# Kernel optimization log

Measured on AMD Instinct MI355X. Metric: run time of the kernel, lower is better.

The kernel has to match this reference:

```python
import jax, jax.numpy as jnp
import numpy as np

CODEBOOK_SIZE = 1024
EMBED_DIM = 256
DECAY = 0.99
EPS = 1e-05


def setup_inputs() -> dict:
    key = jax.random.key(0)
    k_in, k_emb = jax.random.split(key)
    inputs = jax.random.normal(k_in, (128, 16, 16, EMBED_DIM), dtype=jnp.float32)
    embedding = jax.random.normal(k_emb, (CODEBOOK_SIZE, EMBED_DIM), dtype=jnp.float32)
    cluster_size = jnp.zeros((CODEBOOK_SIZE,), dtype=jnp.float32)
    embedding_avg = embedding.copy()
    return {
        "inputs": inputs,
        "embedding": embedding,
        "cluster_size": cluster_size,
        "embedding_avg": embedding_avg,
    }


def reference(inputs, embedding, cluster_size, embedding_avg):
    K, D = embedding.shape
    flat = inputs.reshape(-1, D)  # [N, D]
    distances = (
        jnp.sum(flat * flat, axis=1, keepdims=True)
        - 2.0 * flat @ embedding.T
        + jnp.sum(embedding * embedding, axis=1)
    )
    encoding_indices = jnp.argmin(distances, axis=1)  # [N]
    quantized = embedding[encoding_indices].reshape(inputs.shape)

    # training-mode EMA codebook update (scatter-add instead of dense one-hot)
    counts = jax.ops.segment_sum(
        jnp.ones_like(encoding_indices, dtype=flat.dtype),
        encoding_indices, num_segments=K)  # [K]
    embeds = jax.ops.segment_sum(flat, encoding_indices, num_segments=K)  # [K, D]
    new_cluster_size = cluster_size * DECAY + (1.0 - DECAY) * counts
    new_embedding_avg = embedding_avg * DECAY + (1.0 - DECAY) * embeds
    total = jnp.sum(new_cluster_size)
    normalized = (new_cluster_size + EPS) / (total + K * EPS) * total
    new_embedding = new_embedding_avg / normalized[:, None]

    commitment_loss = jnp.mean(
        (inputs - jax.lax.stop_gradient(quantized)) ** 2)
    # straight-through estimator
    quantized_st = inputs + jax.lax.stop_gradient(quantized - inputs)
    token_ids = encoding_indices.reshape(inputs.shape[:-1])
    return (quantized_st, token_ids, commitment_loss,
            new_embedding, new_cluster_size, new_embedding_avg)
```

## Files before the change

kernel.cpp:

```cpp
#include <hip/hip_runtime.h>

#define NROWS 32768
#define DIM 256
#define KCODES 1024
#define DECAYF 0.99f
#define EPSF 1e-5f

typedef float f32x4 __attribute__((ext_vector_type(4)));
typedef short short8 __attribute__((ext_vector_type(8)));


__device__ inline unsigned short f2bf(float f) {
    unsigned u = __float_as_uint(f);
    return (unsigned short)((u + 0x7FFFu + ((u >> 16) & 1u)) >> 16);
}
__device__ inline float bf2f(unsigned short h) {
    return __uint_as_float(((unsigned)h) << 16);
}

__device__ __forceinline__ void gload_lds16(const void* g, void* l) {
    __builtin_amdgcn_global_load_lds(
        (const __attribute__((address_space(1))) unsigned int*)g,
        (__attribute__((address_space(3))) unsigned int*)l, 16, 0, 0);
}

__global__ __launch_bounds__(256) void k_split2(
    const float* __restrict__ x, const float* __restrict__ emb,
    unsigned short* __restrict__ xh, unsigned short* __restrict__ xm,
    unsigned short* __restrict__ xl, unsigned short* __restrict__ eh,
    unsigned short* __restrict__ em, unsigned short* __restrict__ el,
    float* __restrict__ enorm, unsigned long long* __restrict__ keys,
    int* __restrict__ counts) {
    int b = blockIdx.x, t = threadIdx.x;
    if (b < 4224) {
        const float* src;
        unsigned short *ph, *pm, *pl;
        int i;
        if (b < 4096) { src = x; ph = xh; pm = xm; pl = xl; i = b * 256 + t; }
        else { src = emb; ph = eh; pm = em; pl = el; i = (b - 4096) * 256 + t; }
        const float4* xp = (const float4*)src;
        float4 a = xp[i * 2], c = xp[i * 2 + 1];
        float v[8] = {a.x, a.y, a.z, a.w, c.x, c.y, c.z, c.w};
        short8 H, M, L;
#pragma unroll
        for (int u = 0; u < 8; ++u) {
            unsigned short h = f2bf(v[u]);
            float r1 = v[u] - bf2f(h);
            unsigned short m = f2bf(r1);
            float r2 = r1 - bf2f(m);
            unsigned short lo = f2bf(r2);
            H[u] = (short)h; M[u] = (short)m; L[u] = (short)lo;
        }
        *(short8*)&ph[(size_t)i * 8] = H;
        *(short8*)&pm[(size_t)i * 8] = M;
        *(short8*)&pl[(size_t)i * 8] = L;
        if (b < 128) keys[b * 256 + t] = 0xFFFFFFFFFFFFFFFFull;
        else if (b < 132) counts[(b - 128) * 256 + t] = 0;
    } else {
        int blk = b - 4224;
        int w = t >> 6, lane = t & 63;
        int c = blk * 4 + w;
        const float4 v = *(const float4*)&emb[(size_t)c * DIM + lane * 4];
        float s = v.x * v.x + v.y * v.y + v.z * v.z + v.w * v.w;
#pragma unroll
        for (int m = 32; m; m >>= 1) s += __shfl_xor(s, m, 64);
        if (lane == 0) enorm[c] = s;
    }
}

__global__ __launch_bounds__(256, 3) void k_distm(
    const unsigned short* __restrict__ xh, const unsigned short* __restrict__ xm,
    const unsigned short* __restrict__ xl, const unsigned short* __restrict__ eh,
    const unsigned short* __restrict__ em, const unsigned short* __restrict__ el,
    const float* __restrict__ enorm, unsigned long long* __restrict__ keys) {
    __shared__ unsigned short S[6][4096];

    const int t = threadIdx.x;
    const int l = t & 63, w = t >> 6;
    const int wr = w >> 1, wc = w & 1;
    const int b = blockIdx.x;
    const int logical = (b & 7) * 256 + (b >> 3);
    const int brow = (logical >> 3) * 128;
    const int bcol = (logical & 7) * 128;

    f32x4 acc[4][4] = {};

    const int rlane = l & 15;
    const int klane = (l >> 4) * 8;
    const int sg0 = 2 * w, sg1 = 2 * w + 1;
    const size_t ra0 = (size_t)(brow + sg0 * 16 + rlane) * 256 + klane;
    const size_t ra1 = (size_t)(brow + sg1 * 16 + rlane) * 256 + klane;
    const size_t ca0 = (size_t)(bcol + sg0 * 16 + rlane) * 256 + klane;
    const size_t ca1 = (size_t)(bcol + sg1 * 16 + rlane) * 256 + klane;

    for (int s = 0; s < 8; ++s) {
        const int k0 = s * 32;
        __builtin_amdgcn_s_barrier();
        gload_lds16(&xh[ra0 + k0], &S[0][sg0 * 512]);
        gload_lds16(&xh[ra1 + k0], &S[0][sg1 * 512]);
        gload_lds16(&eh[ca0 + k0], &S[3][sg0 * 512]);
        gload_lds16(&eh[ca1 + k0], &S[3][sg1 * 512]);
        gload_lds16(&em[ca0 + k0], &S[4][sg0 * 512]);
        gload_lds16(&em[ca1 + k0], &S[4][sg1 * 512]);
        gload_lds16(&xm[ra0 + k0], &S[1][sg0 * 512]);
        gload_lds16(&xm[ra1 + k0], &S[1][sg1 * 512]);
        gload_lds16(&el[ca0 + k0], &S[5][sg0 * 512]);
        gload_lds16(&el[ca1 + k0], &S[5][sg1 * 512]);
        gload_lds16(&xl[ra0 + k0], &S[2][sg0 * 512]);
        gload_lds16(&xl[ra1 + k0], &S[2][sg1 * 512]);

        short8 ah[4], bh[4], am[4], bm[4], bl[4], al[4];

        asm volatile("s_waitcnt vmcnt(8)" ::: "memory");
        __builtin_amdgcn_s_barrier();
#pragma unroll
        for (int i = 0; i < 4; ++i)
            ah[i] = *(const short8*)&S[0][(wr * 4 + i) * 512 + l * 8];
#pragma unroll
        for (int j = 0; j < 4; ++j)
            bh[j] = *(const short8*)&S[3][(wc * 4 + j) * 512 + l * 8];
        __builtin_amdgcn_s_setprio(1);
#pragma unroll
        for (int i = 0; i < 4; ++i)
#pragma unroll
            for (int j = 0; j < 4; ++j)
                acc[i][j] = __builtin_amdgcn_mfma_f32_16x16x32_bf16(
                    ah[i], bh[j], acc[i][j], 0, 0, 0);
        __builtin_amdgcn_s_setprio(0);

        asm volatile("s_waitcnt vmcnt(6)" ::: "memory");
        __builtin_amdgcn_s_barrier();
#pragma unroll
        for (int j = 0; j < 4; ++j)
            bm[j] = *(const short8*)&S[4][(wc * 4 + j) * 512 + l * 8];
        __builtin_amdgcn_s_setprio(1);
#pragma unroll
        for (int i = 0; i < 4; ++i)
#pragma unroll
            for (int j = 0; j < 4; ++j)
                acc[i][j] = __builtin_amdgcn_mfma_f32_16x16x32_bf16(
                    ah[i], bm[j], acc[i][j], 0, 0, 0);
        __builtin_amdgcn_s_setprio(0);

        asm volatile("s_waitcnt vmcnt(4)" ::: "memory");
        __builtin_amdgcn_s_barrier();
#pragma unroll
        for (int i = 0; i < 4; ++i)
            am[i] = *(const short8*)&S[1][(wr * 4 + i) * 512 + l * 8];
        __builtin_amdgcn_s_setprio(1);
#pragma unroll
        for (int i = 0; i < 4; ++i)
#pragma unroll
            for (int j = 0; j < 4; ++j)
                acc[i][j] = __builtin_amdgcn_mfma_f32_16x16x32_bf16(
                    am[i], bh[j], acc[i][j], 0, 0, 0);
#pragma unroll
        for (int i = 0; i < 4; ++i)
#pragma unroll
            for (int j = 0; j < 4; ++j)
                acc[i][j] = __builtin_amdgcn_mfma_f32_16x16x32_bf16(
                    am[i], bm[j], acc[i][j], 0, 0, 0);
        __builtin_amdgcn_s_setprio(0);

        asm volatile("s_waitcnt vmcnt(2)" ::: "memory");
        __builtin_amdgcn_s_barrier();
#pragma unroll
        for (int j = 0; j < 4; ++j)
            bl[j] = *(const short8*)&S[5][(wc * 4 + j) * 512 + l * 8];
        __builtin_amdgcn_s_setprio(1);
#pragma unroll
        for (int i = 0; i < 4; ++i)
#pragma unroll
            for (int j = 0; j < 4; ++j)
                acc[i][j] = __builtin_amdgcn_mfma_f32_16x16x32_bf16(
                    ah[i], bl[j], acc[i][j], 0, 0, 0);
        __builtin_amdgcn_s_setprio(0);

        asm volatile("s_waitcnt vmcnt(0)" ::: "memory");
        __builtin_amdgcn_s_barrier();
#pragma unroll
        for (int i = 0; i < 4; ++i)
            al[i] = *(const short8*)&S[2][(wr * 4 + i) * 512 + l * 8];
        __builtin_amdgcn_s_setprio(1);
#pragma unroll
        for (int i = 0; i < 4; ++i)
#pragma unroll
            for (int j = 0; j < 4; ++j)
                acc[i][j] = __builtin_amdgcn_mfma_f32_16x16x32_bf16(
                    al[i], bh[j], acc[i][j], 0, 0, 0);
        __builtin_amdgcn_s_setprio(0);

        asm volatile("s_waitcnt lgkmcnt(0)" ::: "memory");
    }

    float en[4];
    int cidx[4];
#pragma unroll
    for (int j = 0; j < 4; ++j) {
        cidx[j] = bcol + wc * 64 + j * 16 + (l & 15);
        en[j] = enorm[cidx[j]];
    }
#pragma unroll
    for (int i = 0; i < 4; ++i) {
#pragma unroll
        for (int r = 0; r < 4; ++r) {
            float best = 3.0e38f;
            int bi = 0x7FFFFFFF;
#pragma unroll
            for (int j = 0; j < 4; ++j) {
                float d = en[j] - 2.0f * acc[i][j][r];
                if (d < best || (d == best && cidx[j] < bi)) { best = d; bi = cidx[j]; }
            }
#pragma unroll
            for (int m = 1; m < 16; m <<= 1) {
                float d2 = __shfl_xor(best, m, 64);
                int b2 = __shfl_xor(bi, m, 64);
                if (d2 < best || (d2 == best && b2 < bi)) { best = d2; bi = b2; }
            }
            if ((l & 15) == 0) {
                int grow = brow + wr * 64 + i * 16 + (l >> 4) * 4 + r;
                unsigned int fb = __float_as_uint(best);
                unsigned int key32 = (fb & 0x80000000u) ? ~fb : (fb | 0x80000000u);
                atomicMin(&keys[grow],
                          ((unsigned long long)key32 << 32) | (unsigned)bi);
            }
        }
    }
}

__global__ __launch_bounds__(256) void k_scatter(const float* __restrict__ x,
                                                 const float* __restrict__ e,
                                                 const unsigned long long* __restrict__ keys,
                                                 float* __restrict__ out_q,
                                                 float* __restrict__ out_tok,
                                                 int* __restrict__ counts,
                                                 float* __restrict__ loss_part) {
    __shared__ float lred[4];
    int w = threadIdx.x >> 6, lane = threadIdx.x & 63;
    int n = blockIdx.x * 4 + w;
    int k = (int)(unsigned int)(keys[n] & 0xFFFFFFFFull);

    size_t xo = (size_t)n * DIM + lane * 4;
    size_t eo = (size_t)k * DIM + lane * 4;
    const float4 xv = *(const float4*)&x[xo];
    const float4 ev = *(const float4*)&e[eo];

    float4 q;
    q.x = xv.x + (ev.x - xv.x);
    q.y = xv.y + (ev.y - xv.y);
    q.z = xv.z + (ev.z - xv.z);
    q.w = xv.w + (ev.w - xv.w);
    *(float4*)&out_q[xo] = q;

    float dx = xv.x - ev.x, dy = xv.y - ev.y, dz = xv.z - ev.z, dw = xv.w - ev.w;
    float ls = dx * dx + dy * dy + dz * dz + dw * dw;
#pragma unroll
    for (int m = 32; m; m >>= 1) ls += __shfl_xor(ls, m, 64);
    if (lane == 0) {
        lred[w] = ls;
        atomicAdd(&counts[k], 1);
        out_tok[n] = (float)k;
    }

    __syncthreads();
    if (threadIdx.x == 0)
        loss_part[blockIdx.x] = lred[0] + lred[1] + lred[2] + lred[3];
}

__global__ __launch_bounds__(1024) void k_mid(const float* __restrict__ cs,
                                              const int* __restrict__ counts,
                                              const float* __restrict__ loss_part,
                                              float* __restrict__ out_loss,
                                              float* __restrict__ out_ncs,
                                              float* __restrict__ ws_total,
                                              int* __restrict__ offsets,
                                              int* __restrict__ cursor) {
    __shared__ float red[1024];
    __shared__ int si[1024];
    int t = threadIdx.x;

    float ls = 0.0f;
    for (int i = t; i < 8192; i += 1024) ls += loss_part[i];
    red[t] = ls;
    __syncthreads();
    for (int s = 512; s; s >>= 1) {
        if (t < s) red[t] += red[t + s];
        __syncthreads();
    }
    if (t == 0) out_loss[0] = red[0] / 8388608.0f;
    __syncthreads();

    float ncs = cs[t] * DECAYF + (1.0f - DECAYF) * (float)counts[t];
    out_ncs[t] = ncs;
    red[t] = ncs;
    __syncthreads();
    for (int s = 512; s; s >>= 1) {
        if (t < s) red[t] += red[t + s];
        __syncthreads();
    }
    if (t == 0) ws_total[0] = red[0];
    __syncthreads();

    int c = counts[t];
    si[t] = c;
    __syncthreads();
    for (int off = 1; off < 1024; off <<= 1) {
        int v = (t >= off) ? si[t - off] : 0;
        __syncthreads();
        si[t] += v;
        __syncthreads();
    }
    int excl = si[t] - c;
    offsets[t] = excl;
    cursor[t] = excl;
}

__global__ __launch_bounds__(256) void k_bucket(const unsigned long long* __restrict__ keys,
                                                int* __restrict__ cursor,
                                                int* __restrict__ bucket) {
    int n = blockIdx.x * 256 + threadIdx.x;
    int k = (int)(unsigned int)(keys[n] & 0xFFFFFFFFull);
    int slot = atomicAdd(&cursor[k], 1);
    bucket[slot] = n;
}

__global__ __launch_bounds__(256) void k_embpart(
    const float* __restrict__ x, const int* __restrict__ bucket,
    const int* __restrict__ offsets, const int* __restrict__ counts,
    float* __restrict__ partial) {
    __shared__ float lds[4][256];
    int k = blockIdx.x >> 2, s = blockIdx.x & 3;
    int w = threadIdx.x >> 6, lane = threadIdx.x & 63;
    int off = offsets[k], cnt = counts[k];
    int qcnt = (cnt + 3) >> 2;
    int start = off + s * qcnt;
    int lim = s * qcnt + qcnt;
    if (lim > cnt) lim = cnt;
    int end = off + lim;

    f32x4 acc = {0.0f, 0.0f, 0.0f, 0.0f};
    int i = start + w;
    for (; i + 12 < end; i += 16) {
        int r0 = bucket[i], r1 = bucket[i + 4], r2 = bucket[i + 8], r3 = bucket[i + 12];
        f32x4 v0 = *(const f32x4*)&x[(size_t)r0 * DIM + lane * 4];
        f32x4 v1 = *(const f32x4*)&x[(size_t)r1 * DIM + lane * 4];
        f32x4 v2 = *(const f32x4*)&x[(size_t)r2 * DIM + lane * 4];
        f32x4 v3 = *(const f32x4*)&x[(size_t)r3 * DIM + lane * 4];
        acc += v0; acc += v1; acc += v2; acc += v3;
    }
    for (; i < end; i += 4)
        acc += *(const f32x4*)&x[(size_t)bucket[i] * DIM + lane * 4];

    *(f32x4*)&lds[w][lane * 4] = acc;
    __syncthreads();
    int d = threadIdx.x;
    float sum = lds[0][d] + lds[1][d] + lds[2][d] + lds[3][d];
    partial[((size_t)s * KCODES + k) * DIM + d] = sum;
}

__global__ __launch_bounds__(256) void k_embfin2(
    const float* __restrict__ partial, const float* __restrict__ avg,
    const float* __restrict__ out_ncs, const float* __restrict__ ws_total,
    float* __restrict__ out_emb, float* __restrict__ out_avg) {
    int k = blockIdx.x, d = threadIdx.x;
    size_t o = (size_t)k * DIM + d;
    float sum = partial[(0 * KCODES + k) * DIM + d]
              + partial[(1 * KCODES + k) * DIM + d]
              + partial[(2 * KCODES + k) * DIM + d]
              + partial[(3 * KCODES + k) * DIM + d];

    float total = ws_total[0];
    float ncs = out_ncs[k];
    float normalized = (ncs + EPSF) / (total + (float)KCODES * EPSF) * total;

    float na = avg[o] * DECAYF + (1.0f - DECAYF) * sum;
    out_avg[o] = na;
    out_emb[o] = na / normalized;
}

extern "C" void kernel_launch(void* const* d_in, const int* in_sizes, int n_in,
                              void* d_out, int out_size, void* d_ws, size_t ws_size,
                              hipStream_t stream) {
    const float* x   = (const float*)d_in[0];
    const float* emb = (const float*)d_in[1];
    const float* cs  = (const float*)d_in[2];
    const float* avg = (const float*)d_in[3];

    float* out      = (float*)d_out;
    float* out_q    = out;
    float* out_tok  = out + 8388608;
    float* out_loss = out + 8421376;
    float* out_emb  = out + 8421377;
    float* out_ncs  = out + 8683521;
    float* out_avg  = out + 8684545;

    char* ws = (char*)d_ws;
    unsigned short* xh = (unsigned short*)(ws + 0);
    unsigned short* xm = (unsigned short*)(ws + 16777216);
    unsigned short* xl = (unsigned short*)(ws + 33554432);
    float* partial   = (float*)(ws + 0);
    unsigned short* eh = (unsigned short*)(ws + 50331648);
    unsigned short* em = (unsigned short*)(ws + 50855936);
    unsigned short* el = (unsigned short*)(ws + 51380224);
    unsigned long long* keys = (unsigned long long*)(ws + 51904512);
    int* counts      = (int*)(ws + 52166656);
    int* offsets     = (int*)(ws + 52170752);
    int* cursor      = (int*)(ws + 52174848);
    int* bucket      = (int*)(ws + 52178944);
    float* loss_part = (float*)(ws + 52310016);
    float* enorm     = (float*)(ws + 52342784);
    float* ws_total  = (float*)(ws + 52346880);

    k_split2<<<4480, 256, 0, stream>>>(x, emb, xh, xm, xl, eh, em, el,
                                       enorm, keys, counts);
    k_distm<<<2048, 256, 0, stream>>>(xh, xm, xl, eh, em, el, enorm, keys);
    k_scatter<<<NROWS / 4, 256, 0, stream>>>(x, emb, keys, out_q, out_tok,
                                             counts, loss_part);
    k_mid<<<1, 1024, 0, stream>>>(cs, counts, loss_part, out_loss, out_ncs,
                                  ws_total, offsets, cursor);
    k_bucket<<<NROWS / 256, 256, 0, stream>>>(keys, cursor, bucket);
    k_embpart<<<KCODES * 4, 256, 0, stream>>>(x, bucket, offsets, counts,
                                              partial);
    k_embfin2<<<KCODES, 256, 0, stream>>>(partial, avg, out_ncs, ws_total,
                                          out_emb, out_avg);
}
```

Baseline: 202.4 us.

## Enlarge distance GEMM block tile to 256x128 with 8 waves

```diff
diff --git a/kernel.cpp b/kernel.cpp
--- a/kernel.cpp
+++ b/kernel.cpp
@@ -68,57 +68,54 @@
     }
 }
 
-__global__ __launch_bounds__(256, 3) void k_distm(
+__global__ __launch_bounds__(512, 4) void k_distm(
     const unsigned short* __restrict__ xh, const unsigned short* __restrict__ xm,
     const unsigned short* __restrict__ xl, const unsigned short* __restrict__ eh,
     const unsigned short* __restrict__ em, const unsigned short* __restrict__ el,
     const float* __restrict__ enorm, unsigned long long* __restrict__ keys) {
-    __shared__ unsigned short S[6][4096];
+    __shared__ unsigned short SA[3][8192];
+    __shared__ unsigned short SB[3][4096];
 
     const int t = threadIdx.x;
     const int l = t & 63, w = t >> 6;
     const int wr = w >> 1, wc = w & 1;
     const int b = blockIdx.x;
-    const int logical = (b & 7) * 256 + (b >> 3);
-    const int brow = (logical >> 3) * 128;
+    const int logical = (b & 7) * 128 + (b >> 3);
+    const int brow = (logical >> 3) * 256;
     const int bcol = (logical & 7) * 128;
 
     f32x4 acc[4][4] = {};
 
     const int rlane = l & 15;
     const int klane = (l >> 4) * 8;
-    const int sg0 = 2 * w, sg1 = 2 * w + 1;
-    const size_t ra0 = (size_t)(brow + sg0 * 16 + rlane) * 256 + klane;
-    const size_t ra1 = (size_t)(brow + sg1 * 16 + rlane) * 256 + klane;
-    const size_t ca0 = (size_t)(bcol + sg0 * 16 + rlane) * 256 + klane;
-    const size_t ca1 = (size_t)(bcol + sg1 * 16 + rlane) * 256 + klane;
+    const size_t rA0 = (size_t)(brow + (2 * w) * 16 + rlane) * 256 + klane;
+    const size_t rA1 = rA0 + 16 * 256;
+    const size_t rB  = (size_t)(bcol + w * 16 + rlane) * 256 + klane;
+    const int sA0 = (2 * w) * 512, sA1 = (2 * w + 1) * 512, sBo = w * 512;
 
     for (int s = 0; s < 8; ++s) {
         const int k0 = s * 32;
         __builtin_amdgcn_s_barrier();
-        gload_lds16(&xh[ra0 + k0], &S[0][sg0 * 512]);
-        gload_lds16(&xh[ra1 + k0], &S[0][sg1 * 512]);
-        gload_lds16(&eh[ca0 + k0], &S[3][sg0 * 512]);
-        gload_lds16(&eh[ca1 + k0], &S[3][sg1 * 512]);
-        gload_lds16(&em[ca0 + k0], &S[4][sg0 * 512]);
-        gload_lds16(&em[ca1 + k0], &S[4][sg1 * 512]);
-        gload_lds16(&xm[ra0 + k0], &S[1][sg0 * 512]);
-        gload_lds16(&xm[ra1 + k0], &S[1][sg1 * 512]);
-        gload_lds16(&el[ca0 + k0], &S[5][sg0 * 512]);
-        gload_lds16(&el[ca1 + k0], &S[5][sg1 * 512]);
-        gload_lds16(&xl[ra0 + k0], &S[2][sg0 * 512]);
-        gload_lds16(&xl[ra1 + k0], &S[2][sg1 * 512]);
+        gload_lds16(&xh[rA0 + k0], &SA[0][sA0]);
+        gload_lds16(&xh[rA1 + k0], &SA[0][sA1]);
+        gload_lds16(&eh[rB + k0],  &SB[0][sBo]);
+        gload_lds16(&em[rB + k0],  &SB[1][sBo]);
+        gload_lds16(&xm[rA0 + k0], &SA[1][sA0]);
+        gload_lds16(&xm[rA1 + k0], &SA[1][sA1]);
+        gload_lds16(&el[rB + k0],  &SB[2][sBo]);
+        gload_lds16(&xl[rA0 + k0], &SA[2][sA0]);
+        gload_lds16(&xl[rA1 + k0], &SA[2][sA1]);
 
         short8 ah[4], bh[4], am[4], bm[4], bl[4], al[4];
 
-        asm volatile("s_waitcnt vmcnt(8)" ::: "memory");
-        __builtin_amdgcn_s_barrier();
-#pragma unroll
-        for (int i = 0; i < 4; ++i)
-            ah[i] = *(const short8*)&S[0][(wr * 4 + i) * 512 + l * 8];
+        asm volatile("s_waitcnt vmcnt(6)" ::: "memory");
+        __builtin_amdgcn_s_barrier();
+#pragma unroll
+        for (int i = 0; i < 4; ++i)
+            ah[i] = *(const short8*)&SA[0][(wr * 4 + i) * 512 + l * 8];
 #pragma unroll
         for (int j = 0; j < 4; ++j)
-            bh[j] = *(const short8*)&S[3][(wc * 4 + j) * 512 + l * 8];
+            bh[j] = *(const short8*)&SB[0][(wc * 4 + j) * 512 + l * 8];
         __builtin_amdgcn_s_setprio(1);
 #pragma unroll
         for (int i = 0; i < 4; ++i)
@@ -128,11 +125,11 @@
                     ah[i], bh[j], acc[i][j], 0, 0, 0);
         __builtin_amdgcn_s_setprio(0);
 
-        asm volatile("s_waitcnt vmcnt(6)" ::: "memory");
+        asm volatile("s_waitcnt vmcnt(5)" ::: "memory");
         __builtin_amdgcn_s_barrier();
 #pragma unroll
         for (int j = 0; j < 4; ++j)
-            bm[j] = *(const short8*)&S[4][(wc * 4 + j) * 512 + l * 8];
+            bm[j] = *(const short8*)&SB[1][(wc * 4 + j) * 512 + l * 8];
         __builtin_amdgcn_s_setprio(1);
 #pragma unroll
         for (int i = 0; i < 4; ++i)
@@ -142,11 +139,11 @@
                     ah[i], bm[j], acc[i][j], 0, 0, 0);
         __builtin_amdgcn_s_setprio(0);
 
-        asm volatile("s_waitcnt vmcnt(4)" ::: "memory");
-        __builtin_amdgcn_s_barrier();
-#pragma unroll
-        for (int i = 0; i < 4; ++i)
-            am[i] = *(const short8*)&S[1][(wr * 4 + i) * 512 + l * 8];
+        asm volatile("s_waitcnt vmcnt(3)" ::: "memory");
+        __builtin_amdgcn_s_barrier();
+#pragma unroll
+        for (int i = 0; i < 4; ++i)
+            am[i] = *(const short8*)&SA[1][(wr * 4 + i) * 512 + l * 8];
         __builtin_amdgcn_s_setprio(1);
 #pragma unroll
         for (int i = 0; i < 4; ++i)
@@ -166,7 +163,7 @@
         __builtin_amdgcn_s_barrier();
 #pragma unroll
         for (int j = 0; j < 4; ++j)
-            bl[j] = *(const short8*)&S[5][(wc * 4 + j) * 512 + l * 8];
+            bl[j] = *(const short8*)&SB[2][(wc * 4 + j) * 512 + l * 8];
         __builtin_amdgcn_s_setprio(1);
 #pragma unroll
         for (int i = 0; i < 4; ++i)
@@ -180,7 +177,7 @@
         __builtin_amdgcn_s_barrier();
 #pragma unroll
         for (int i = 0; i < 4; ++i)
-            al[i] = *(const short8*)&S[2][(wr * 4 + i) * 512 + l * 8];
+            al[i] = *(const short8*)&SA[2][(wr * 4 + i) * 512 + l * 8];
         __builtin_amdgcn_s_setprio(1);
 #pragma unroll
         for (int i = 0; i < 4; ++i)
@@ -413,7 +410,7 @@
 
     k_split2<<<4480, 256, 0, stream>>>(x, emb, xh, xm, xl, eh, em, el,
                                        enorm, keys, counts);
-    k_distm<<<2048, 256, 0, stream>>>(xh, xm, xl, eh, em, el, enorm, keys);
+    k_distm<<<1024, 512, 0, stream>>>(xh, xm, xl, eh, em, el, enorm, keys);
     k_scatter<<<NROWS / 4, 256, 0, stream>>>(x, emb, keys, out_q, out_tok,
                                              counts, loss_part);
     k_mid<<<1, 1024, 0, stream>>>(cs, counts, loss_part, out_loss, out_ncs,
```

After: 255.8 us. +26.4%, slower.

## Double-buffer input tiles in LDS to prefetch next k-step during distance GEMM

Applied to the files above, without the earlier changes.

```diff
diff --git a/kernel.cpp b/kernel.cpp
--- a/kernel.cpp
+++ b/kernel.cpp
@@ -73,7 +73,8 @@
     const unsigned short* __restrict__ xl, const unsigned short* __restrict__ eh,
     const unsigned short* __restrict__ em, const unsigned short* __restrict__ el,
     const float* __restrict__ enorm, unsigned long long* __restrict__ keys) {
-    __shared__ unsigned short S[6][4096];
+    __shared__ unsigned short EA[3][4096];
+    __shared__ unsigned short XA[2][3][4096];
 
     const int t = threadIdx.x;
     const int l = t & 63, w = t >> 6;
@@ -92,33 +93,46 @@
     const size_t ra1 = (size_t)(brow + sg1 * 16 + rlane) * 256 + klane;
     const size_t ca0 = (size_t)(bcol + sg0 * 16 + rlane) * 256 + klane;
     const size_t ca1 = (size_t)(bcol + sg1 * 16 + rlane) * 256 + klane;
+    const int lo0 = sg0 * 512, lo1 = sg1 * 512;
+
+    gload_lds16(&xh[ra0], &XA[0][0][lo0]);
+    gload_lds16(&xh[ra1], &XA[0][0][lo1]);
+    gload_lds16(&xm[ra0], &XA[0][1][lo0]);
+    gload_lds16(&xm[ra1], &XA[0][1][lo1]);
+    gload_lds16(&xl[ra0], &XA[0][2][lo0]);
+    gload_lds16(&xl[ra1], &XA[0][2][lo1]);
 
     for (int s = 0; s < 8; ++s) {
         const int k0 = s * 32;
+        const int cur = s & 1;
         __builtin_amdgcn_s_barrier();
-        gload_lds16(&xh[ra0 + k0], &S[0][sg0 * 512]);
-        gload_lds16(&xh[ra1 + k0], &S[0][sg1 * 512]);
-        gload_lds16(&eh[ca0 + k0], &S[3][sg0 * 512]);
-        gload_lds16(&eh[ca1 + k0], &S[3][sg1 * 512]);
-        gload_lds16(&em[ca0 + k0], &S[4][sg0 * 512]);
-        gload_lds16(&em[ca1 + k0], &S[4][sg1 * 512]);
-        gload_lds16(&xm[ra0 + k0], &S[1][sg0 * 512]);
-        gload_lds16(&xm[ra1 + k0], &S[1][sg1 * 512]);
-        gload_lds16(&el[ca0 + k0], &S[5][sg0 * 512]);
-        gload_lds16(&el[ca1 + k0], &S[5][sg1 * 512]);
-        gload_lds16(&xl[ra0 + k0], &S[2][sg0 * 512]);
-        gload_lds16(&xl[ra1 + k0], &S[2][sg1 * 512]);
+        gload_lds16(&eh[ca0 + k0], &EA[0][lo0]);
+        gload_lds16(&eh[ca1 + k0], &EA[0][lo1]);
+        gload_lds16(&em[ca0 + k0], &EA[1][lo0]);
+        gload_lds16(&em[ca1 + k0], &EA[1][lo1]);
+        gload_lds16(&el[ca0 + k0], &EA[2][lo0]);
+        gload_lds16(&el[ca1 + k0], &EA[2][lo1]);
+        if (s < 7) {
+            const int kn = k0 + 32;
+            gload_lds16(&xh[ra0 + kn], &XA[cur ^ 1][0][lo0]);
+            gload_lds16(&xh[ra1 + kn], &XA[cur ^ 1][0][lo1]);
+            gload_lds16(&xm[ra0 + kn], &XA[cur ^ 1][1][lo0]);
+            gload_lds16(&xm[ra1 + kn], &XA[cur ^ 1][1][lo1]);
+            gload_lds16(&xl[ra0 + kn], &XA[cur ^ 1][2][lo0]);
+            gload_lds16(&xl[ra1 + kn], &XA[cur ^ 1][2][lo1]);
+        }
 
         short8 ah[4], bh[4], am[4], bm[4], bl[4], al[4];
 
-        asm volatile("s_waitcnt vmcnt(8)" ::: "memory");
+        if (s < 7) asm volatile("s_waitcnt vmcnt(10)" ::: "memory");
+        else       asm volatile("s_waitcnt vmcnt(4)" ::: "memory");
         __builtin_amdgcn_s_barrier();
 #pragma unroll
         for (int i = 0; i < 4; ++i)
-            ah[i] = *(const short8*)&S[0][(wr * 4 + i) * 512 + l * 8];
+            ah[i] = *(const short8*)&XA[cur][0][(wr * 4 + i) * 512 + l * 8];
 #pragma unroll
         for (int j = 0; j < 4; ++j)
-            bh[j] = *(const short8*)&S[3][(wc * 4 + j) * 512 + l * 8];
+            bh[j] = *(const short8*)&EA[0][(wc * 4 + j) * 512 + l * 8];
         __builtin_amdgcn_s_setprio(1);
 #pragma unroll
         for (int i = 0; i < 4; ++i)
@@ -128,11 +142,12 @@
                     ah[i], bh[j], acc[i][j], 0, 0, 0);
         __builtin_amdgcn_s_setprio(0);
 
-        asm volatile("s_waitcnt vmcnt(6)" ::: "memory");
+        if (s < 7) asm volatile("s_waitcnt vmcnt(8)" ::: "memory");
+        else       asm volatile("s_waitcnt vmcnt(2)" ::: "memory");
         __builtin_amdgcn_s_barrier();
 #pragma unroll
         for (int j = 0; j < 4; ++j)
-            bm[j] = *(const short8*)&S[4][(wc * 4 + j) * 512 + l * 8];
+            bm[j] = *(const short8*)&EA[1][(wc * 4 + j) * 512 + l * 8];
         __builtin_amdgcn_s_setprio(1);
 #pragma unroll
         for (int i = 0; i < 4; ++i)
@@ -142,11 +157,9 @@
                     ah[i], bm[j], acc[i][j], 0, 0, 0);
         __builtin_amdgcn_s_setprio(0);
 
-        asm volatile("s_waitcnt vmcnt(4)" ::: "memory");
-        __builtin_amdgcn_s_barrier();
-#pragma unroll
-        for (int i = 0; i < 4; ++i)
-            am[i] = *(const short8*)&S[1][(wr * 4 + i) * 512 + l * 8];
+#pragma unroll
+        for (int i = 0; i < 4; ++i)
+            am[i] = *(const short8*)&XA[cur][1][(wr * 4 + i) * 512 + l * 8];
         __builtin_amdgcn_s_setprio(1);
 #pragma unroll
         for (int i = 0; i < 4; ++i)
@@ -162,11 +175,12 @@
                     am[i], bm[j], acc[i][j], 0, 0, 0);
         __builtin_amdgcn_s_setprio(0);
 
-        asm volatile("s_waitcnt vmcnt(2)" ::: "memory");
+        if (s < 7) asm volatile("s_waitcnt vmcnt(6)" ::: "memory");
+        else       asm volatile("s_waitcnt vmcnt(0)" ::: "memory");
         __builtin_amdgcn_s_barrier();
 #pragma unroll
         for (int j = 0; j < 4; ++j)
-            bl[j] = *(const short8*)&S[5][(wc * 4 + j) * 512 + l * 8];
+            bl[j] = *(const short8*)&EA[2][(wc * 4 + j) * 512 + l * 8];
         __builtin_amdgcn_s_setprio(1);
 #pragma unroll
         for (int i = 0; i < 4; ++i)
@@ -176,11 +190,9 @@
                     ah[i], bl[j], acc[i][j], 0, 0, 0);
         __builtin_amdgcn_s_setprio(0);
 
-        asm volatile("s_waitcnt vmcnt(0)" ::: "memory");
-        __builtin_amdgcn_s_barrier();
-#pragma unroll
-        for (int i = 0; i < 4; ++i)
-            al[i] = *(const short8*)&S[2][(wr * 4 + i) * 512 + l * 8];
+#pragma unroll
+        for (int i = 0; i < 4; ++i)
+            al[i] = *(const short8*)&XA[cur][2][(wr * 4 + i) * 512 + l * 8];
         __builtin_amdgcn_s_setprio(1);
 #pragma unroll
         for (int i = 0; i < 4; ++i)
```

After: 230.8 us. +14.0%, slower.
